# Kernel optimization log

Measured on AMD Instinct MI355X. Metric: run time of the kernel, lower is better.

## Reference

```python
import jax, jax.numpy as jnp
import numpy as np

EPS = 1e-05

def exp_map_at_origin(v, c):
    sqrt_c = jnp.sqrt(c)
    v_norm = jnp.maximum(jnp.linalg.norm(v, axis=-1, keepdims=True), EPS)
    return (1.0 / sqrt_c) * jnp.tanh(sqrt_c * v_norm) * (v / v_norm)

def log_map_at_origin(y, c):
    sqrt_c = jnp.sqrt(c)
    y_norm = jnp.maximum(jnp.linalg.norm(y, axis=-1, keepdims=True), EPS)
    y_norm_clamped = jnp.minimum(y_norm, 1.0 / sqrt_c - EPS)
    return (1.0 / sqrt_c) * jnp.arctanh(sqrt_c * y_norm_clamped) * (y / y_norm)

def poincare_distance(x, y, c):
    # x, y: [B, H, S, d]; returns [B, H, S, S]
    sqrt_c = jnp.sqrt(c)
    xns = jnp.sum(x * x, axis=-1, keepdims=True)          # [B,H,S,1]
    yns = jnp.sum(y * y, axis=-1, keepdims=True)          # [B,H,S,1]
    xy = jnp.einsum('bhsd,bhtd->bhst', x, y)
    xnsb = xns                                            # broadcast over t
    ynsb = jnp.swapaxes(yns, -2, -1)                      # [B,H,1,S]
    diff_norm_sq = xnsb - 2.0 * xy + ynsb
    denom = jnp.maximum((1.0 - c * xnsb) * (1.0 - c * ynsb), EPS)
    arg = jnp.maximum(1.0 + 2.0 * c * diff_norm_sq / denom, 1.0 + EPS)
    return (1.0 / sqrt_c) * jnp.arccosh(arg)

def setup_inputs() -> dict:
    key = jax.random.key(0)
    ks = jax.random.split(key, 5)
    B, S, D = 2, 1024, 1024
    x = jax.random.normal(ks[0], (B, S, D), dtype=jnp.float32)
    scale = 0.02
    W_q = scale * jax.random.normal(ks[1], (D, D), dtype=jnp.float32)
    W_k = scale * jax.random.normal(ks[2], (D, D), dtype=jnp.float32)
    W_v = scale * jax.random.normal(ks[3], (D, D), dtype=jnp.float32)
    W_o = scale * jax.random.normal(ks[4], (D, D), dtype=jnp.float32)
    return {
        'x': x, 'W_q': W_q, 'W_k': W_k, 'W_v': W_v, 'W_o': W_o,
        'log_c': jnp.zeros((), jnp.float32),
        'beta': jnp.zeros((), jnp.float32),
        'attention_bias': jnp.zeros((), jnp.float32),
    }

def reference(x, W_q, W_k, W_v, W_o, log_c, beta, attention_bias):
    B, S, D = x.shape
    H = 16
    dh = D // H
    c = jax.nn.softplus(log_c)
    beta_pos = jax.nn.softplus(beta)

    def split_heads(t):  # [B,S,D] -> [B,H,S,dh]
        return jnp.transpose(t.reshape(B, S, H, dh), (0, 2, 1, 3))

    q_t = split_heads(x @ W_q.T)
    k_t = split_heads(x @ W_k.T)
    v_t = split_heads(x @ W_v.T)

    q_h = exp_map_at_origin(q_t, c)
    k_h = exp_map_at_origin(k_t, c)
    v_h = exp_map_at_origin(v_t, c)

    dist = poincare_distance(q_h, k_h, c)                 # [B,H,S,S]
    scores = -beta_pos * dist - attention_bias
    weights = jax.nn.softmax(scores, axis=-1)

    v_tan = log_map_at_origin(v_h, c)
    out_tan = jnp.einsum('bhst,bhtd->bhsd', weights, v_tan)
    out_hyp = exp_map_at_origin(out_tan, c)
    out_heads_tan = log_map_at_origin(out_hyp, c)

    concat = jnp.transpose(out_heads_tan, (0, 2, 1, 3)).reshape(B, S, D)
    return concat @ W_o.T
```

## Files before the change

### kernel.cpp

```cpp
#include <hip/hip_runtime.h>
#include <math.h>


#define EPS_ 1e-5f

constexpr int Ss = 1024, Dd = 1024, Hh = 16, DHh = 64;

typedef __attribute__((ext_vector_type(8))) short bf16x8;
typedef __attribute__((ext_vector_type(4))) short s16x4;
typedef __attribute__((ext_vector_type(4))) float f32x4;

__device__ __forceinline__ float softplusf_(float x) {
    return (x > 20.f) ? x : log1pf(expf(x));
}
__device__ __forceinline__ float waveSum64(float v) {
#pragma unroll
    for (int m = 32; m >= 1; m >>= 1) v += __shfl_xor(v, m, 64);
    return v;
}
__device__ __forceinline__ short f2bf(float f) {
    union { float f; unsigned u; } v; v.f = f;
    unsigned r = v.u + 0x7FFFu + ((v.u >> 16) & 1u);
    return (short)(r >> 16);
}
__device__ __forceinline__ float bf2f(unsigned short h) {
    union { unsigned u; float f; } v; v.u = ((unsigned)h) << 16;
    return v.f;
}
__device__ __forceinline__ unsigned pks(short a, short b) {
    return (unsigned)(unsigned short)a | ((unsigned)(unsigned short)b << 16);
}

#if __has_builtin(__builtin_amdgcn_cvt_pk_bf16_f32)
typedef __attribute__((ext_vector_type(2))) __bf16 bfp2;
__device__ __forceinline__ unsigned cvtpk(float a, float b) {
    union { bfp2 v; unsigned u; } x;
    x.v = __builtin_amdgcn_cvt_pk_bf16_f32(a, b);
    return x.u;
}
#else
__device__ __forceinline__ unsigned cvtpk(float a, float b) { return pks(f2bf(a), f2bf(b)); }
#endif

#if __has_builtin(__builtin_amdgcn_sqrtf)
#define FSQRT __builtin_amdgcn_sqrtf
#else
#define FSQRT sqrtf
#endif
#if __has_builtin(__builtin_amdgcn_logf)
#define FLOG2 __builtin_amdgcn_logf
#else
#define FLOG2 __log2f
#endif
#if __has_builtin(__builtin_amdgcn_exp2f)
#define FEXP2 __builtin_amdgcn_exp2f
#else
#define FEXP2 exp2f
#endif

__global__ __launch_bounds__(256) void split_all(
    const float* __restrict__ x,  const float* __restrict__ Wq,
    const float* __restrict__ Wk, const float* __restrict__ Wv,
    const float* __restrict__ Wo,
    short* __restrict__ xh,  short* __restrict__ wqh,
    short* __restrict__ wkh, short* __restrict__ wvh, short* __restrict__ woh)
{
    int g = blockIdx.x * 256 + threadIdx.x;
    const float* src; short* dst; int base;
    if (g < 524288)       { src = x;  dst = xh;  base = g; }
    else if (g < 786432)  { src = Wq; dst = wqh; base = g - 524288; }
    else if (g < 1048576) { src = Wk; dst = wkh; base = g - 786432; }
    else if (g < 1310720) { src = Wv; dst = wvh; base = g - 1048576; }
    else                  { src = Wo; dst = woh; base = g - 1310720; }
    float4 v = *(const float4*)(src + (size_t)base * 4);
    uint2 hp; hp.x = cvtpk(v.x, v.y); hp.y = cvtpk(v.z, v.w);
    *(uint2*)(dst + (size_t)base * 4) = hp;
}

__global__ __launch_bounds__(256, 6) void gemm_qkv(
    const short* __restrict__ Ap,
    const short* __restrict__ Wq, const short* __restrict__ Wk, const short* __restrict__ Wv,
    short* __restrict__ qh, short* __restrict__ kh, short* __restrict__ vtT,
    float* __restrict__ qnsT, float2* __restrict__ knpk,
    const float* __restrict__ p_logc)
{
    const int z = blockIdx.z;
    const short* Bp = (z == 0) ? Wq : (z == 1 ? Wk : Wv);
    const int K = 1024;

    __shared__ short As[64 * 72];
    __shared__ short Bs[64 * 72];

    const int tid = threadIdx.x;
    const int wv = tid >> 6, lane = tid & 63, quad = lane >> 4, l15 = lane & 15;
    const int bm = blockIdx.y * 64, bn = blockIdx.x * 64;
    const int sr = tid >> 2, sq = (tid & 3) * 16;

    const short* gA = Ap + (size_t)(bm + sr) * K + sq;
    const short* gB = Bp + (size_t)(bn + sr) * K + sq;

    f32x4 acc[4];
#pragma unroll
    for (int j = 0; j < 4; j++) acc[j] = (f32x4){0.f, 0.f, 0.f, 0.f};

    bf16x8 a0 = *(const bf16x8*)gA;
    bf16x8 a1 = *(const bf16x8*)(gA + 8);
    bf16x8 b0 = *(const bf16x8*)gB;
    bf16x8 b1 = *(const bf16x8*)(gB + 8);

    for (int k0 = 0; k0 < K; k0 += 64) {
        __syncthreads();
        *(bf16x8*)&As[sr * 72 + sq]     = a0;
        *(bf16x8*)&As[sr * 72 + sq + 8] = a1;
        *(bf16x8*)&Bs[sr * 72 + sq]     = b0;
        *(bf16x8*)&Bs[sr * 72 + sq + 8] = b1;
        __syncthreads();
        if (k0 + 64 < K) {
            a0 = *(const bf16x8*)(gA + k0 + 64);
            a1 = *(const bf16x8*)(gA + k0 + 64 + 8);
            b0 = *(const bf16x8*)(gB + k0 + 64);
            b1 = *(const bf16x8*)(gB + k0 + 64 + 8);
        }
#pragma unroll
        for (int w = 0; w < 2; w++) {
            bf16x8 fa = *(const bf16x8*)&As[(wv * 16 + l15) * 72 + w * 32 + quad * 8];
#pragma unroll
            for (int nt = 0; nt < 4; nt++) {
                bf16x8 fb = *(const bf16x8*)&Bs[(nt * 16 + l15) * 72 + w * 32 + quad * 8];
                acc[nt] = __builtin_amdgcn_mfma_f32_16x16x32_bf16(fa, fb, acc[nt], 0, 0, 0);
            }
        }
    }

    const float c = softplusf_(p_logc[0]);
    const float sc = sqrtf(c);
    const float twoC = 2.f * c;
    const int h0 = blockIdx.x;
    const int mbase = bm + wv * 16;

    if (z < 2) {
        short* yout = (z == 0) ? qh : kh;
        float fr[4];
#pragma unroll
        for (int r = 0; r < 4; r++) {
            float s2 = 0.f;
#pragma unroll
            for (int nt = 0; nt < 4; nt++) s2 += acc[nt][r] * acc[nt][r];
#pragma unroll
            for (int mk = 1; mk < 16; mk <<= 1) s2 += __shfl_xor(s2, mk, 64);
            float n = fmaxf(sqrtf(s2), EPS_);
            float fac = tanhf(sc * n) / (sc * n);
            fr[r] = fac;
            if (l15 == 0) {
                int m = mbase + quad * 4 + r;
                int bI = m >> 10, s = m & 1023;
                float yns = s2 * fac * fac;
                if (z == 0) {
                    qnsT[(size_t)(bI * Hh + h0) * Ss + s] = yns;
                } else {
                    knpk[(size_t)(bI * Hh + h0) * Ss + s]
                        = make_float2(yns, twoC / (1.f - c * yns));
                }
            }
        }
#pragma unroll
        for (int nt = 0; nt < 4; nt++)
#pragma unroll
            for (int r = 0; r < 4; r++) {
                int m = mbase + quad * 4 + r;
                yout[(size_t)m * Dd + bn + nt * 16 + l15] = f2bf(acc[nt][r] * fr[r]);
            }
    } else {
        float tr[4];
#pragma unroll
        for (int r = 0; r < 4; r++) {
            float s2 = 0.f;
#pragma unroll
            for (int nt = 0; nt < 4; nt++) s2 += acc[nt][r] * acc[nt][r];
#pragma unroll
            for (int mk = 1; mk < 16; mk <<= 1) s2 += __shfl_xor(s2, mk, 64);
            float n = fmaxf(sqrtf(s2), EPS_);
            float fac = tanhf(sc * n) / (sc * n);
            float yn = n * fac;
            float ycl = fminf(yn, 1.f / sc - EPS_);
            float f2 = atanhf(sc * ycl) / (sc * fmaxf(yn, EPS_));
            tr[r] = fac * f2;
        }
        const int m0 = mbase + quad * 4;
        const int bI = m0 >> 10, s0 = m0 & 1023;
#pragma unroll
        for (int nt = 0; nt < 4; nt++) {
            int d = nt * 16 + l15;
            uint2 pk;
            pk.x = cvtpk(acc[nt][0] * tr[0], acc[nt][1] * tr[1]);
            pk.y = cvtpk(acc[nt][2] * tr[2], acc[nt][3] * tr[3]);
            *(uint2*)&vtT[((size_t)(bI * Hh + h0) * DHh + d) * Ss + s0] = pk;
        }
    }
}

__global__ __launch_bounds__(256) void attn_mfma(
    const short* __restrict__ qh, const short* __restrict__ kh, const short* __restrict__ vtT,
    const float* __restrict__ qnsT, const float2* __restrict__ knpk,
    unsigned short* __restrict__ Opart, float* __restrict__ lpart,
    const float* __restrict__ p_logc, const float* __restrict__ p_beta)
{
    const float c = softplusf_(p_logc[0]);
    const float sc = sqrtf(c);
    const float bp = softplusf_(p_beta[0]);
    const float nkc = -bp / sc;
    const float cap = 2.f * c * 1e5f;
    const float onePlus = 1.f + EPS_;

    const int h = blockIdx.y, b = blockIdx.z;
    const int kr = blockIdx.x & 3, qt = blockIdx.x >> 2;
    const int tid = threadIdx.x;
    const int wv = tid >> 6, lane = tid & 63;
    const int quad = lane >> 4, l15 = lane & 15;
    const int bh = b * Hh + h;
    const int q = qt * 64 + wv * 16 + l15;

    __shared__ short Ks[64][72];
    __shared__ short Vt[64][72];

    const short* qb = qh + (size_t)(b * Ss + q) * Dd + h * DHh + quad * 8;
    bf16x8 qf0 = *(const bf16x8*)qb;
    bf16x8 qf1 = *(const bf16x8*)(qb + 32);

    const float qn = qnsT[(size_t)bh * Ss + q];
    const float irq = 1.f / (1.f - c * qn);

    f32x4 O4[4];
#pragma unroll
    for (int nt = 0; nt < 4; nt++) O4[nt] = (f32x4){0.f, 0.f, 0.f, 0.f};
    float lac = 0.f;

    const int tbase = kr * 256;
    const int sr = tid >> 2, sseg = (tid & 3) * 16;
    const short* kgp = kh + (size_t)(b * Ss + tbase + sr) * Dd + h * DHh + sseg;
    const short* vgp = vtT + ((size_t)bh * DHh + sr) * Ss + tbase + sseg;
    const float2* nb = knpk + (size_t)bh * Ss;

    bf16x8 kA0 = *(const bf16x8*)kgp;
    bf16x8 kA1 = *(const bf16x8*)(kgp + 8);
    bf16x8 vA0 = *(const bf16x8*)vgp;
    bf16x8 vA1 = *(const bf16x8*)(vgp + 8);

    for (int ch = 0; ch < 4; ch++) {
        const int t0 = tbase + ch * 64;

        __syncthreads();
        *(bf16x8*)&Ks[sr][sseg]     = kA0;
        *(bf16x8*)&Ks[sr][sseg + 8] = kA1;
        *(bf16x8*)&Vt[sr][sseg]     = vA0;
        *(bf16x8*)&Vt[sr][sseg + 8] = vA1;
        __syncthreads();

        if (ch < 3) {
            kA0 = *(const bf16x8*)(kgp + (size_t)((ch + 1) * 64) * Dd);
            kA1 = *(const bf16x8*)(kgp + (size_t)((ch + 1) * 64) * Dd + 8);
            vA0 = *(const bf16x8*)(vgp + (ch + 1) * 64);
            vA1 = *(const bf16x8*)(vgp + (ch + 1) * 64 + 8);
        }

        f32x4 acc[4];
#pragma unroll
        for (int nt = 0; nt < 4; nt++) {
            bf16x8 k0 = *(const bf16x8*)&Ks[nt * 16 + l15][quad * 8];
            bf16x8 k1 = *(const bf16x8*)&Ks[nt * 16 + l15][32 + quad * 8];
            f32x4 a = (f32x4){0.f, 0.f, 0.f, 0.f};
            a = __builtin_amdgcn_mfma_f32_16x16x32_bf16(k0, qf0, a, 0, 0, 0);
            a = __builtin_amdgcn_mfma_f32_16x16x32_bf16(k1, qf1, a, 0, 0, 0);
            acc[nt] = a;
        }

        float sv[4][4];
#pragma unroll
        for (int nt = 0; nt < 4; nt++) {
            const float2* np = nb + t0 + nt * 16 + quad * 4;
            f32x4 n0 = *(const f32x4*)np;
            f32x4 n1 = *(const f32x4*)(np + 2);
#pragma unroll
            for (int r = 0; r < 4; r++) {
                float kn   = (r < 2) ? n0[(r & 1) * 2]     : n1[(r & 1) * 2];
                float ik2c = (r < 2) ? n0[(r & 1) * 2 + 1] : n1[(r & 1) * 2 + 1];
                float dns = (qn + kn) - 2.f * acc[nt][r];
                float co  = fminf(irq * ik2c, cap);
                float arg = fmaxf(fmaf(co, dns, 1.f), onePlus);
                float u   = arg + FSQRT(fmaf(arg, arg, -1.f));
                float p   = FEXP2(nkc * FLOG2(u));
                sv[nt][r] = p;
                lac += p;
            }
        }

        union { unsigned u[4]; bf16x8 v; } p0, p1;
        p0.u[0] = cvtpk(sv[0][0], sv[0][1]); p0.u[1] = cvtpk(sv[0][2], sv[0][3]);
        p0.u[2] = cvtpk(sv[1][0], sv[1][1]); p0.u[3] = cvtpk(sv[1][2], sv[1][3]);
        p1.u[0] = cvtpk(sv[2][0], sv[2][1]); p1.u[1] = cvtpk(sv[2][2], sv[2][3]);
        p1.u[2] = cvtpk(sv[3][0], sv[3][1]); p1.u[3] = cvtpk(sv[3][2], sv[3][3]);

#pragma unroll
        for (int nt = 0; nt < 4; nt++) {
            const short* vr = &Vt[nt * 16 + l15][quad * 4];
            s16x4 a0 = *(const s16x4*)(vr);
            s16x4 a1 = *(const s16x4*)(vr + 16);
            s16x4 a2 = *(const s16x4*)(vr + 32);
            s16x4 a3 = *(const s16x4*)(vr + 48);
            bf16x8 v0 = __builtin_shufflevector(a0, a1, 0, 1, 2, 3, 4, 5, 6, 7);
            bf16x8 v1 = __builtin_shufflevector(a2, a3, 0, 1, 2, 3, 4, 5, 6, 7);
            O4[nt] = __builtin_amdgcn_mfma_f32_16x16x32_bf16(v0, p0.v, O4[nt], 0, 0, 0);
            O4[nt] = __builtin_amdgcn_mfma_f32_16x16x32_bf16(v1, p1.v, O4[nt], 0, 0, 0);
        }
    }

    lac += __shfl_xor(lac, 16, 64);
    lac += __shfl_xor(lac, 32, 64);
    unsigned short* ob = Opart + (((size_t)bh * 4 + kr) * Ss + q) * DHh;
#pragma unroll
    for (int nt = 0; nt < 4; nt++) {
        uint2 pk;
        pk.x = cvtpk(O4[nt][0], O4[nt][1]);
        pk.y = cvtpk(O4[nt][2], O4[nt][3]);
        *(uint2*)(ob + nt * 16 + quad * 4) = pk;
    }
    if (lane < 16)
        lpart[((size_t)bh * 4 + kr) * Ss + qt * 64 + wv * 16 + lane] = lac;
}

__global__ __launch_bounds__(256) void attn_combine(
    const unsigned short* __restrict__ Opart, const float* __restrict__ lpart,
    short* __restrict__ ccb, const float* __restrict__ p_logc)
{
    const float c = softplusf_(p_logc[0]);
    const float sc = sqrtf(c);
    const int wv = threadIdx.x >> 6, d = threadIdx.x & 63;
    const int task = blockIdx.x * 4 + wv;
    const int bh = task >> 10, s = task & 1023;

    float O = 0.f, l = 0.f;
#pragma unroll
    for (int k = 0; k < 4; k++) {
        O += bf2f(Opart[(((size_t)bh * 4 + k) * Ss + s) * DHh + d]);
        l += lpart[((size_t)bh * 4 + k) * Ss + s];
    }
    float ot = O / l;

    float t2 = waveSum64(ot * ot);
    float n = fmaxf(sqrtf(t2), EPS_);
    float fac = tanhf(sc * n) / (sc * n);
    float y2 = t2 * fac * fac;
    float yn = fmaxf(sqrtf(y2), EPS_);
    float ycl = fminf(yn, 1.f / sc - EPS_);
    float fac2 = atanhf(sc * ycl) / (sc * yn);
    float tot = fac * fac2;

    int b = bh >> 4, hh = bh & 15;
    ccb[(size_t)(b * Ss + s) * Dd + hh * DHh + d] = f2bf(ot * tot);
}

__global__ __launch_bounds__(256, 6) void gemm_out(
    const short* __restrict__ Ap, const short* __restrict__ Bp,
    float* __restrict__ Cp)
{
    const int K = 1024, N = 1024;
    __shared__ short As[64 * 72];
    __shared__ short Bs[64 * 72];
    const int tid = threadIdx.x;
    const int wv = tid >> 6, lane = tid & 63, quad = lane >> 4, l15 = lane & 15;
    const int bm = blockIdx.y * 64, bn = blockIdx.x * 64;
    const int sr = tid >> 2, sq = (tid & 3) * 16;

    const short* gA = Ap + (size_t)(bm + sr) * K + sq;
    const short* gB = Bp + (size_t)(bn + sr) * K + sq;

    f32x4 acc[4];
#pragma unroll
    for (int j = 0; j < 4; j++) acc[j] = (f32x4){0.f, 0.f, 0.f, 0.f};

    bf16x8 a0 = *(const bf16x8*)gA;
    bf16x8 a1 = *(const bf16x8*)(gA + 8);
    bf16x8 b0 = *(const bf16x8*)gB;
    bf16x8 b1 = *(const bf16x8*)(gB + 8);

    for (int k0 = 0; k0 < K; k0 += 64) {
        __syncthreads();
        *(bf16x8*)&As[sr * 72 + sq]     = a0;
        *(bf16x8*)&As[sr * 72 + sq + 8] = a1;
        *(bf16x8*)&Bs[sr * 72 + sq]     = b0;
        *(bf16x8*)&Bs[sr * 72 + sq + 8] = b1;
        __syncthreads();
        if (k0 + 64 < K) {
            a0 = *(const bf16x8*)(gA + k0 + 64);
            a1 = *(const bf16x8*)(gA + k0 + 64 + 8);
            b0 = *(const bf16x8*)(gB + k0 + 64);
            b1 = *(const bf16x8*)(gB + k0 + 64 + 8);
        }
#pragma unroll
        for (int w = 0; w < 2; w++) {
            bf16x8 fa = *(const bf16x8*)&As[(wv * 16 + l15) * 72 + w * 32 + quad * 8];
#pragma unroll
            for (int nt = 0; nt < 4; nt++) {
                bf16x8 fb = *(const bf16x8*)&Bs[(nt * 16 + l15) * 72 + w * 32 + quad * 8];
                acc[nt] = __builtin_amdgcn_mfma_f32_16x16x32_bf16(fa, fb, acc[nt], 0, 0, 0);
            }
        }
    }
#pragma unroll
    for (int nt = 0; nt < 4; nt++)
#pragma unroll
        for (int r = 0; r < 4; r++)
            Cp[(size_t)(bm + wv * 16 + quad * 4 + r) * N + bn + nt * 16 + l15] = acc[nt][r];
}

extern "C" void kernel_launch(void* const* d_in, const int* in_sizes, int n_in,
                              void* d_out, int out_size, void* d_ws, size_t ws_size,
                              hipStream_t stream)
{
    const float* x    = (const float*)d_in[0];
    const float* Wq   = (const float*)d_in[1];
    const float* Wk   = (const float*)d_in[2];
    const float* Wv   = (const float*)d_in[3];
    const float* Wo   = (const float*)d_in[4];
    const float* logc = (const float*)d_in[5];
    const float* beta = (const float*)d_in[6];
    float* out = (float*)d_out;

    const size_t M2 = 2097152, M1 = 1048576;
    short* ws    = (short*)d_ws;
    short* xh    = ws;
    short* wqh   = xh + M2;
    short* wkh   = wqh + M1;
    short* wvh   = wkh + M1;
    short* woh   = wvh + M1;
    short* qh    = woh + M1;
    short* kh    = qh + M2;
    short* vtT   = kh + M2;
    float* qnsT  = (float*)(vtT + M2);
    float2* knpk = (float2*)(qnsT + 32768);
    float* lpart = (float*)(knpk + 32768);
    unsigned short* Opart = (unsigned short*)(lpart + 131072);
    short* ccb   = xh;

    split_all<<<dim3(6144), 256, 0, stream>>>(x, Wq, Wk, Wv, Wo, xh, wqh, wkh, wvh, woh);
    gemm_qkv<<<dim3(16, 32, 3), 256, 0, stream>>>(xh, wqh, wkh, wvh,
        qh, kh, vtT, qnsT, knpk, logc);
    attn_mfma<<<dim3(64, 16, 2), 256, 0, stream>>>(qh, kh, vtT, qnsT, knpk,
        Opart, lpart, logc, beta);
    attn_combine<<<dim3(8192), 256, 0, stream>>>(Opart, lpart, ccb, logc);
    gemm_out<<<dim3(16, 32), 256, 0, stream>>>(ccb, woh, out);
}
```

Before: 181.4 us.

## Double-buffer K/V shared tiles and pre-permute V layout for vector LDS reads

```diff
diff --git a/kernel.cpp b/kernel.cpp
--- a/kernel.cpp
+++ b/kernel.cpp
@@ -220,8 +220,8 @@
     const int bh = b * Hh + h;
     const int q = qt * 64 + wv * 16 + l15;
 
-    __shared__ short Ks[64][72];
-    __shared__ short Vt[64][72];
+    __shared__ short Ks[2][64][72];
+    __shared__ short Vt[2][64][72];
 
     const short* qb = qh + (size_t)(b * Ss + q) * Dd + h * DHh + quad * 8;
     bf16x8 qf0 = *(const bf16x8*)qb;
@@ -237,6 +237,8 @@
 
     const int tbase = kr * 256;
     const int sr = tid >> 2, sseg = (tid & 3) * 16;
+    const int vhi = sseg & 32;
+    const int vup = (sseg & 16) ? 4 : 0;
     const short* kgp = kh + (size_t)(b * Ss + tbase + sr) * Dd + h * DHh + sseg;
     const short* vgp = vtT + ((size_t)bh * DHh + sr) * Ss + tbase + sseg;
     const float2* nb = knpk + (size_t)bh * Ss;
@@ -245,16 +247,20 @@
     bf16x8 kA1 = *(const bf16x8*)(kgp + 8);
     bf16x8 vA0 = *(const bf16x8*)vgp;
     bf16x8 vA1 = *(const bf16x8*)(vgp + 8);
+    {
+        *(bf16x8*)&Ks[0][sr][sseg]     = kA0;
+        *(bf16x8*)&Ks[0][sr][sseg + 8] = kA1;
+        short* vrow = &Vt[0][sr][0];
+        *(s16x4*)(vrow + vhi + vup)      = __builtin_shufflevector(vA0, vA0, 0, 1, 2, 3);
+        *(s16x4*)(vrow + vhi + 8 + vup)  = __builtin_shufflevector(vA0, vA0, 4, 5, 6, 7);
+        *(s16x4*)(vrow + vhi + 16 + vup) = __builtin_shufflevector(vA1, vA1, 0, 1, 2, 3);
+        *(s16x4*)(vrow + vhi + 24 + vup) = __builtin_shufflevector(vA1, vA1, 4, 5, 6, 7);
+    }
+    __syncthreads();
 
     for (int ch = 0; ch < 4; ch++) {
+        const int cur = ch & 1, nxt = cur ^ 1;
         const int t0 = tbase + ch * 64;
-
-        __syncthreads();
-        *(bf16x8*)&Ks[sr][sseg]     = kA0;
-        *(bf16x8*)&Ks[sr][sseg + 8] = kA1;
-        *(bf16x8*)&Vt[sr][sseg]     = vA0;
-        *(bf16x8*)&Vt[sr][sseg + 8] = vA1;
-        __syncthreads();
 
         if (ch < 3) {
             kA0 = *(const bf16x8*)(kgp + (size_t)((ch + 1) * 64) * Dd);
@@ -263,11 +269,19 @@
             vA1 = *(const bf16x8*)(vgp + (ch + 1) * 64 + 8);
         }
 
+        f32x4 n0[4], n1[4];
+#pragma unroll
+        for (int nt = 0; nt < 4; nt++) {
+            const float2* np = nb + t0 + nt * 16 + quad * 4;
+            n0[nt] = *(const f32x4*)np;
+            n1[nt] = *(const f32x4*)(np + 2);
+        }
+
         f32x4 acc[4];
 #pragma unroll
         for (int nt = 0; nt < 4; nt++) {
-            bf16x8 k0 = *(const bf16x8*)&Ks[nt * 16 + l15][quad * 8];
-            bf16x8 k1 = *(const bf16x8*)&Ks[nt * 16 + l15][32 + quad * 8];
+            bf16x8 k0 = *(const bf16x8*)&Ks[cur][nt * 16 + l15][quad * 8];
+            bf16x8 k1 = *(const bf16x8*)&Ks[cur][nt * 16 + l15][32 + quad * 8];
             f32x4 a = (f32x4){0.f, 0.f, 0.f, 0.f};
             a = __builtin_amdgcn_mfma_f32_16x16x32_bf16(k0, qf0, a, 0, 0, 0);
             a = __builtin_amdgcn_mfma_f32_16x16x32_bf16(k1, qf1, a, 0, 0, 0);
@@ -277,13 +291,10 @@
         float sv[4][4];
 #pragma unroll
         for (int nt = 0; nt < 4; nt++) {
-            const float2* np = nb + t0 + nt * 16 + quad * 4;
-            f32x4 n0 = *(const f32x4*)np;
-            f32x4 n1 = *(const f32x4*)(np + 2);
 #pragma unroll
             for (int r = 0; r < 4; r++) {
-                float kn   = (r < 2) ? n0[(r & 1) * 2]     : n1[(r & 1) * 2];
-                float ik2c = (r < 2) ? n0[(r & 1) * 2 + 1] : n1[(r & 1) * 2 + 1];
+                float kn   = (r < 2) ? n0[nt][(r & 1) * 2]     : n1[nt][(r & 1) * 2];
+                float ik2c = (r < 2) ? n0[nt][(r & 1) * 2 + 1] : n1[nt][(r & 1) * 2 + 1];
                 float dns = (qn + kn) - 2.f * acc[nt][r];
                 float co  = fminf(irq * ik2c, cap);
                 float arg = fmaxf(fmaf(co, dns, 1.f), onePlus);
@@ -302,15 +313,21 @@
 
 #pragma unroll
         for (int nt = 0; nt < 4; nt++) {
-            const short* vr = &Vt[nt * 16 + l15][quad * 4];
-            s16x4 a0 = *(const s16x4*)(vr);
-            s16x4 a1 = *(const s16x4*)(vr + 16);
-            s16x4 a2 = *(const s16x4*)(vr + 32);
-            s16x4 a3 = *(const s16x4*)(vr + 48);
-            bf16x8 v0 = __builtin_shufflevector(a0, a1, 0, 1, 2, 3, 4, 5, 6, 7);
-            bf16x8 v1 = __builtin_shufflevector(a2, a3, 0, 1, 2, 3, 4, 5, 6, 7);
+            bf16x8 v0 = *(const bf16x8*)&Vt[cur][nt * 16 + l15][quad * 8];
+            bf16x8 v1 = *(const bf16x8*)&Vt[cur][nt * 16 + l15][32 + quad * 8];
             O4[nt] = __builtin_amdgcn_mfma_f32_16x16x32_bf16(v0, p0.v, O4[nt], 0, 0, 0);
             O4[nt] = __builtin_amdgcn_mfma_f32_16x16x32_bf16(v1, p1.v, O4[nt], 0, 0, 0);
+        }
+
+        if (ch < 3) {
+            *(bf16x8*)&Ks[nxt][sr][sseg]     = kA0;
+            *(bf16x8*)&Ks[nxt][sr][sseg + 8] = kA1;
+            short* vrow = &Vt[nxt][sr][0];
+            *(s16x4*)(vrow + vhi + vup)      = __builtin_shufflevector(vA0, vA0, 0, 1, 2, 3);
+            *(s16x4*)(vrow + vhi + 8 + vup)  = __builtin_shufflevector(vA0, vA0, 4, 5, 6, 7);
+            *(s16x4*)(vrow + vhi + 16 + vup) = __builtin_shufflevector(vA1, vA1, 0, 1, 2, 3);
+            *(s16x4*)(vrow + vhi + 24 + vup) = __builtin_shufflevector(vA1, vA1, 4, 5, 6, 7);
+            __syncthreads();
         }
     }
 
```

New measurement: 180.0 us. Within noise of the previous version (-0.7%).
